# Optimization experiments

Hardware: AMD Instinct MI355X
Metric: run time of the kernel (lower is better)

Reference implementation:

```python
import jax, jax.numpy as jnp
import numpy as np
from jax import lax

NK, NV, DK, DV, K, C = 16, 32, 128, 128, 4, 2048
KEY_DIM = NK * DK
VAL_DIM = NV * DV
CONV_DIM = 2 * KEY_DIM + VAL_DIM
EPS = 1e-6


def setup_inputs() -> dict:
    key = jax.random.key(0)
    ks = jax.random.split(key, 10)
    B, T = 2, 2048
    s = 0.02
    return {
        "x": jax.random.normal(ks[0], (B, T, C), jnp.float32),
        "input_pos": jnp.arange(T, dtype=jnp.int32),
        "W_qkv": jax.random.normal(ks[1], (CONV_DIM, C), jnp.float32) * s,
        "W_z": jax.random.normal(ks[2], (VAL_DIM, C), jnp.float32) * s,
        "W_b": jax.random.normal(ks[3], (NV, C), jnp.float32) * s,
        "W_a": jax.random.normal(ks[4], (NV, C), jnp.float32) * s,
        "conv_w": jax.random.normal(ks[5], (CONV_DIM, 1, K), jnp.float32) * 0.1,
        "dt_bias": jnp.ones((NV,), jnp.float32),
        "A_log": jnp.log(jax.random.uniform(ks[6], (NV,), jnp.float32, 1e-3, 16.0)),
        "norm_w": jnp.ones((DV,), jnp.float32),
        "W_out": jax.random.normal(ks[7], (C, VAL_DIM), jnp.float32) * s,
        "conv_state": jnp.zeros((B, CONV_DIM, K), jnp.float32),
        "recurrent_state": jnp.zeros((B, NV, DK, DV), jnp.float32),
    }


def reference(x, input_pos, W_qkv, W_z, W_b, W_a, conv_w, dt_bias, A_log,
              norm_w, W_out, conv_state, recurrent_state):
    B, T, _ = x.shape
    # reset cached state when starting a new sequence (input_pos[0] == 0)
    keep = 1.0 - (input_pos[0] == 0).astype(x.dtype)
    conv_state = conv_state * keep
    state0 = recurrent_state * keep

    qkv = jnp.einsum('btc,dc->btd', x, W_qkv)                      # [B,T,CONV_DIM]
    z = jnp.einsum('btc,dc->btd', x, W_z).reshape(B, T, NV, DV)
    beta = jax.nn.sigmoid(jnp.einsum('btc,hc->bth', x, W_b))       # [B,T,NV]
    a = jnp.einsum('btc,hc->bth', x, W_a)
    g = -jnp.exp(A_log) * jax.nn.softplus(a + dt_bias)             # [B,T,NV]

    # causal depthwise conv using cached conv_state as left context
    conv_in = jnp.concatenate([conv_state, qkv.transpose(0, 2, 1)], axis=-1)  # [B,D,K+T]
    conv_out = lax.conv_general_dilated(
        conv_in, conv_w, (1,), 'VALID',
        dimension_numbers=('NCH', 'OIH', 'NCH'),
        feature_group_count=CONV_DIM)
    qkv_c = jax.nn.silu(conv_out[:, :, -T:]).transpose(0, 2, 1)    # [B,T,CONV_DIM]

    q = qkv_c[..., :KEY_DIM].reshape(B, T, NK, DK)
    k = qkv_c[..., KEY_DIM:2 * KEY_DIM].reshape(B, T, NK, DK)
    v = qkv_c[..., 2 * KEY_DIM:].reshape(B, T, NV, DV)
    q = q / jnp.maximum(jnp.linalg.norm(q, axis=-1, keepdims=True), 1e-12)
    k = k / jnp.maximum(jnp.linalg.norm(k, axis=-1, keepdims=True), 1e-12)
    rep = NV // NK
    if rep > 1:
        q = jnp.repeat(q, rep, axis=2)
        k = jnp.repeat(k, rep, axis=2)

    # gated delta-rule recurrence over time
    def step(carry, xs):
        q_i, k_i, v_i, g_i, b_i = xs                               # [B,H,*]
        new = (jnp.exp(g_i)[..., None, None] * carry
               + b_i[..., None, None] * (k_i[..., :, None] * v_i[..., None, :]))
        out = jnp.einsum('bhk,bhkv->bhv', q_i, new)
        return new, out

    xs = (q.transpose(1, 0, 2, 3), k.transpose(1, 0, 2, 3),
          v.transpose(1, 0, 2, 3), g.transpose(1, 0, 2), beta.transpose(1, 0, 2))
    state, outs = lax.scan(step, state0, xs)
    o = outs.transpose(1, 0, 2, 3)                                 # [B,T,NV,DV]

    # gated RMSNorm (Mamba2-style): gate with silu(z), then RMS-normalize
    o = o * jax.nn.silu(z)
    var = jnp.mean(o * o, axis=-1, keepdims=True)
    o = o * lax.rsqrt(var + EPS) * norm_w
    return jnp.einsum('btd,cd->btc', o.reshape(B, T, VAL_DIM), W_out)
```

## Files before the change

### kernel.cpp

```cpp
#include <hip/hip_runtime.h>
#include <hip/hip_bf16.h>
#include <math.h>

#define NKH 16
#define NVH 32
#define DKD 128
#define DVD 128
#define CDIM 2048
#define KEY_DIM 2048
#define VAL_DIM 4096
#define CONV_DIM 8192
#define BB 2
#define TT 2048
#define MROWS 4096
#define CH 64
#define NCHUNK 32

typedef unsigned short u16;
typedef __bf16 bf16x8 __attribute__((ext_vector_type(8)));
typedef float f32x4 __attribute__((ext_vector_type(4)));

__device__ __forceinline__ u16 f2bf(float f) {
    union { float f; unsigned u; } a; a.f = f;
    unsigned u = a.u;
    u += 0x7fffu + ((u >> 16) & 1u);
    return (u16)(u >> 16);
}
__device__ __forceinline__ float bf2f(u16 h) {
    union { unsigned u; float f; } a; a.u = ((unsigned)h) << 16;
    return a.f;
}
union BF8 { bf16x8 v; uint2 u2[2]; uint4 u4; u16 s[8]; };
__device__ __forceinline__ bf16x8 lds_ld8(const u16* p) {
    BF8 t; t.u2[0] = *(const uint2*)p; t.u2[1] = *(const uint2*)(p + 4); return t.v;
}
__device__ __forceinline__ void lds_st8(u16* p, uint4 v) {
    *(uint2*)p = make_uint2(v.x, v.y); *(uint2*)(p + 4) = make_uint2(v.z, v.w);
}

__global__ __launch_bounds__(256) void fill_kernel(float* __restrict__ p, float v, int n) {
    int i = blockIdx.x * 256 + threadIdx.x;
    if (i < n) p[i] = v;
}

__global__ __launch_bounds__(256) void cast_kernel(const float* __restrict__ src,
                                                   u16* __restrict__ dst, int n4) {
    int i = blockIdx.x * 256 + threadIdx.x;
    if (i >= n4) return;
    float4 v = ((const float4*)src)[i];
    ushort4 r;
    r.x = f2bf(v.x); r.y = f2bf(v.y); r.z = f2bf(v.z); r.w = f2bf(v.w);
    ((ushort4*)dst)[i] = r;
}

template<int OUT_BF16>
__global__ __launch_bounds__(256) void gemm_nt(const u16* __restrict__ A,
                                               const u16* __restrict__ Bm,
                                               void* __restrict__ Cv,
                                               int M, int N, int K) {
    __shared__ __align__(16) u16 As[128 * 64];
    __shared__ __align__(16) u16 Bs[128 * 64];
    const int tid  = threadIdx.x;
    const int lane = tid & 63;
    const int wave = tid >> 6;
    const int m0 = blockIdx.y * 128;
    const int n0 = blockIdx.x * 128;
    const int wm = (wave & 1) * 64;
    const int wn = (wave >> 1) * 64;
    const int l15  = lane & 15;
    const int quad = lane >> 4;

    f32x4 acc[4][4];
#pragma unroll
    for (int i = 0; i < 4; ++i)
#pragma unroll
        for (int j = 0; j < 4; ++j) acc[i][j] = (f32x4)0.0f;

    const int crow = tid >> 3;
    const int ccol = (tid & 7) * 8;

    for (int k0 = 0; k0 < K; k0 += 64) {
#pragma unroll
        for (int p = 0; p < 4; ++p) {
            int row = p * 32 + crow;
            const u16* ga = A + (size_t)(m0 + row) * K + k0 + ccol;
            char* la = (char*)As + (size_t)(p * 256 + (wave << 6)) * 16;
            __builtin_amdgcn_global_load_lds((const __attribute__((address_space(1))) void*)ga,
                                             (__attribute__((address_space(3))) void*)la, 16, 0, 0);
            const u16* gb = Bm + (size_t)(n0 + row) * K + k0 + ccol;
            char* lb = (char*)Bs + (size_t)(p * 256 + (wave << 6)) * 16;
            __builtin_amdgcn_global_load_lds((const __attribute__((address_space(1))) void*)gb,
                                             (__attribute__((address_space(3))) void*)lb, 16, 0, 0);
        }
        __syncthreads();
#pragma unroll
        for (int kk = 0; kk < 64; kk += 32) {
            bf16x8 af[4], bfr[4];
#pragma unroll
            for (int i = 0; i < 4; ++i) {
                af[i]  = *(const bf16x8*)&As[(wm + i * 16 + l15) * 64 + kk + quad * 8];
                bfr[i] = *(const bf16x8*)&Bs[(wn + i * 16 + l15) * 64 + kk + quad * 8];
            }
#pragma unroll
            for (int i = 0; i < 4; ++i)
#pragma unroll
                for (int j = 0; j < 4; ++j)
                    acc[i][j] = __builtin_amdgcn_mfma_f32_16x16x32_bf16(af[i], bfr[j], acc[i][j], 0, 0, 0);
        }
        __syncthreads();
    }
#pragma unroll
    for (int i = 0; i < 4; ++i) {
#pragma unroll
        for (int j = 0; j < 4; ++j) {
#pragma unroll
            for (int r = 0; r < 4; ++r) {
                int grow = m0 + wm + i * 16 + quad * 4 + r;
                int gcol = n0 + wn + j * 16 + l15;
                if (OUT_BF16) {
                    ((u16*)Cv)[(size_t)grow * N + gcol] = f2bf(acc[i][j][r]);
                } else {
                    ((float*)Cv)[(size_t)grow * N + gcol] = acc[i][j][r];
                }
            }
        }
    }
}

__global__ __launch_bounds__(256) void bg_epilogue(const float* __restrict__ scores,
                                                   const float* __restrict__ dt_bias,
                                                   const float* __restrict__ A_log,
                                                   float* __restrict__ beta,
                                                   float* __restrict__ g) {
    int i = blockIdx.x * 256 + threadIdx.x;
    int row = i >> 6, col = i & 63;
    float s = scores[(size_t)row * 128 + col];
    if (col < 32) {
        beta[(size_t)row * 32 + col] = 1.f / (1.f + __expf(-s));
    } else {
        int h = col - 32;
        float aa = s + dt_bias[h];
        float sp = (aa > 20.f) ? aa : log1pf(__expf(aa));
        g[(size_t)row * 32 + h] = -__expf(A_log[h]) * sp;
    }
}

__global__ __launch_bounds__(256) void conv_silu_kernel(const u16* __restrict__ qkv,
                                                        const float* __restrict__ conv_w,
                                                        const float* __restrict__ conv_state,
                                                        const int* __restrict__ input_pos,
                                                        u16* __restrict__ qkvc) {
    const int d   = blockIdx.x * 256 + threadIdx.x;
    const int row = blockIdx.y;
    const int t   = row & (TT - 1);
    const int b   = row >> 11;
    const float keep = (input_pos[0] == 0) ? 0.f : 1.f;
    float4 w = *(const float4*)&conv_w[(size_t)d * 4];
    float acc = 0.f;
#pragma unroll
    for (int j = 0; j < 4; ++j) {
        int u = t + j - 3;
        float v;
        if (u >= 0) v = bf2f(qkv[(size_t)(b * TT + u) * CONV_DIM + d]);
        else        v = keep * conv_state[((size_t)b * CONV_DIM + d) * 4 + (u + 4)];
        acc += (&w.x)[j] * v;
    }
    float s = acc / (1.f + __expf(-acc));
    qkvc[(size_t)row * CONV_DIM + d] = f2bf(s);
}

__global__ __launch_bounds__(256) void qknorm_kernel(u16* __restrict__ qkvc) {
    const int gid  = blockIdx.x * 4 + (threadIdx.x >> 6);
    const int lane = threadIdx.x & 63;
    const int row  = gid >> 5;
    const int h    = gid & 31;
    u16* p = qkvc + (size_t)row * CONV_DIM + h * 128;
    ushort2 vb = *(ushort2*)&p[lane * 2];
    float v0 = bf2f(vb.x), v1 = bf2f(vb.y);
    float ss = v0 * v0 + v1 * v1;
#pragma unroll
    for (int off = 32; off; off >>= 1) ss += __shfl_xor(ss, off);
    float scale = 1.f / fmaxf(sqrtf(ss), 1e-12f);
    ushort2 r;
    r.x = f2bf(v0 * scale);
    r.y = f2bf(v1 * scale);
    *(ushort2*)&p[lane * 2] = r;
}

__global__ __launch_bounds__(64) void gates_kernel(const float* __restrict__ g,
                                                   const float* __restrict__ beta_,
                                                   float* __restrict__ gcum,
                                                   float* __restrict__ qsb,
                                                   float* __restrict__ wkb,
                                                   float* __restrict__ dLb) {
    const int bh = blockIdx.x, c = blockIdx.y;
    const int b = bh >> 5, h = bh & 31;
    const int t = threadIdx.x;
    const int row = b * TT + c * CH + t;
    float G = g[(size_t)row * 32 + h];
#pragma unroll
    for (int off = 1; off < 64; off <<= 1) {
        float x = __shfl_up(G, off);
        if (t >= off) G += x;
    }
    float GL = __shfl(G, 63);
    int oidx = bh * TT + c * CH + t;
    gcum[oidx] = G;
    qsb[oidx] = __expf(G);
    wkb[oidx] = __expf(GL - G) * beta_[(size_t)row * 32 + h];
    if (t == 0) dLb[bh * NCHUNK + c] = __expf(GL);
}

__global__ __launch_bounds__(256) void ktrans_kernel(const u16* __restrict__ qkvc,
                                                     u16* __restrict__ kT) {
    const int id = blockIdx.x;
    const int tt = id & 31, dkh = (id >> 5) & 1, hk = (id >> 6) & 15, b = id >> 10;
    const int t0 = tt * 64, dk0 = dkh * 64;
    __shared__ __align__(16) u16 tile[64 * 68];
#pragma unroll
    for (int it = 0; it < 2; ++it) {
        int idx = it * 256 + threadIdx.x;
        int tl = idx >> 3, c8 = (idx & 7) * 8;
        uint4 v = *(const uint4*)&qkvc[(size_t)(b * TT + t0 + tl) * CONV_DIM + KEY_DIM + hk * 128 + dk0 + c8];
        lds_st8(&tile[tl * 68 + c8], v);
    }
    __syncthreads();
#pragma unroll
    for (int it = 0; it < 2; ++it) {
        int idx = it * 256 + threadIdx.x;
        int dkl = idx >> 3, t8 = (idx & 7) * 8;
        unsigned w[4];
#pragma unroll
        for (int p = 0; p < 4; ++p) {
            unsigned lo = tile[(t8 + 2 * p) * 68 + dkl];
            unsigned hi = tile[(t8 + 2 * p + 1) * 68 + dkl];
            w[p] = lo | (hi << 16);
        }
        *(uint4*)&kT[((size_t)((b * 16 + hk) * 128 + dk0 + dkl)) * TT + t0 + t8] =
            make_uint4(w[0], w[1], w[2], w[3]);
    }
}

__global__ __launch_bounds__(256) void chunk_state_kernel(const u16* __restrict__ qkvc,
                                                          const u16* __restrict__ kT,
                                                          const float* __restrict__ qsb,
                                                          const float* __restrict__ wkb,
                                                          const float* __restrict__ dLb,
                                                          const float* __restrict__ rec_state,
                                                          const int* __restrict__ input_pos,
                                                          u16* __restrict__ o) {
    const int b = blockIdx.x, h = blockIdx.y, dvs = blockIdx.z;
    const int tid = threadIdx.x, lane = tid & 63, wave = tid >> 6;
    const int l15 = lane & 15, quad = lane >> 4;
    const int hq = h >> 1, bh = b * 32 + h;
    const float keep = (input_pos[0] == 0) ? 0.f : 1.f;

    __shared__ __align__(16) u16 sQ[64 * 132];
    __shared__ __align__(16) u16 sKT[128 * 68];
    __shared__ __align__(16) u16 sR[32 * 132];
    __shared__ float sQS[64];

    f32x4 st[2][2];
#pragma unroll
    for (int i = 0; i < 2; ++i)
#pragma unroll
        for (int j = 0; j < 2; ++j)
#pragma unroll
            for (int r = 0; r < 4; ++r) {
                int dv = dvs * 32 + i * 16 + quad * 4 + r;
                int dk = wave * 32 + j * 16 + l15;
                st[i][j][r] = keep * rec_state[((size_t)(bh * 128 + dk)) * 128 + dv];
            }

    for (int c = 0; c < NCHUNK; ++c) {
        const int t0 = c * CH;
#pragma unroll
        for (int i = 0; i < 2; ++i)
#pragma unroll
            for (int j = 0; j < 2; ++j)
#pragma unroll
                for (int r = 0; r < 4; ++r)
                    sR[(i * 16 + quad * 4 + r) * 132 + wave * 32 + j * 16 + l15] = f2bf(st[i][j][r]);
#pragma unroll
        for (int it = 0; it < 4; ++it) {
            int idx = it * 256 + tid;
            int t = idx >> 4, c8 = (idx & 15) * 8;
            uint4 v = *(const uint4*)&qkvc[(size_t)(b * TT + t0 + t) * CONV_DIM + hq * 128 + c8];
            lds_st8(&sQ[t * 132 + c8], v);
        }
        if (tid < 64) sQS[tid] = qsb[bh * TT + t0 + tid];
        __syncthreads();
        {
            f32x4 ao[2] = {(f32x4)0.0f, (f32x4)0.0f};
#pragma unroll
            for (int kk = 0; kk < 4; ++kk) {
                bf16x8 af = lds_ld8(&sQ[(wave * 16 + l15) * 132 + kk * 32 + quad * 8]);
                bf16x8 b0 = lds_ld8(&sR[(l15) * 132 + kk * 32 + quad * 8]);
                bf16x8 b1 = lds_ld8(&sR[(16 + l15) * 132 + kk * 32 + quad * 8]);
                ao[0] = __builtin_amdgcn_mfma_f32_16x16x32_bf16(af, b0, ao[0], 0, 0, 0);
                ao[1] = __builtin_amdgcn_mfma_f32_16x16x32_bf16(af, b1, ao[1], 0, 0, 0);
            }
#pragma unroll
            for (int j = 0; j < 2; ++j)
#pragma unroll
                for (int r = 0; r < 4; ++r) {
                    int t = wave * 16 + quad * 4 + r;
                    int dv = dvs * 32 + j * 16 + l15;
                    o[((size_t)(b * TT + t0 + t) * 32 + h) * 128 + dv] = f2bf(ao[j][r] * sQS[t]);
                }
        }
        __syncthreads();
#pragma unroll
        for (int it = 0; it < 4; ++it) {
            int idx = it * 256 + tid;
            int dk = idx >> 3, t8 = (idx & 7) * 8;
            uint4 v = *(const uint4*)&kT[((size_t)((b * 16 + hq) * 128 + dk)) * TT + t0 + t8];
            lds_st8(&sKT[dk * 68 + t8], v);
        }
        {
            int t = tid >> 2, dvo = (tid & 3) * 8;
            float w = wkb[bh * TT + t0 + t];
            BF8 v;
            v.u4 = *(const uint4*)&qkvc[(size_t)(b * TT + t0 + t) * CONV_DIM + 2 * KEY_DIM + h * 128 + dvs * 32 + dvo];
#pragma unroll
            for (int u = 0; u < 8; ++u)
                sR[(dvo + u) * 68 + t] = f2bf(bf2f(v.s[u]) * w);
        }
        __syncthreads();
        {
            float d = dLb[bh * NCHUNK + c];
#pragma unroll
            for (int i = 0; i < 2; ++i)
#pragma unroll
                for (int j = 0; j < 2; ++j)
#pragma unroll
                    for (int r = 0; r < 4; ++r) st[i][j][r] *= d;
#pragma unroll
            for (int kk = 0; kk < 2; ++kk) {
                bf16x8 af[2], bfv[2];
#pragma unroll
                for (int i = 0; i < 2; ++i)
                    af[i] = lds_ld8(&sR[(i * 16 + l15) * 68 + kk * 32 + quad * 8]);
#pragma unroll
                for (int j = 0; j < 2; ++j)
                    bfv[j] = lds_ld8(&sKT[(wave * 32 + j * 16 + l15) * 68 + kk * 32 + quad * 8]);
#pragma unroll
                for (int i = 0; i < 2; ++i)
#pragma unroll
                    for (int j = 0; j < 2; ++j)
                        st[i][j] = __builtin_amdgcn_mfma_f32_16x16x32_bf16(af[i], bfv[j], st[i][j], 0, 0, 0);
            }
        }
        __syncthreads();
    }
}

__global__ __launch_bounds__(256) void chunk_intra_kernel(const u16* __restrict__ qkvc,
                                                          const float* __restrict__ gcum,
                                                          const float* __restrict__ beta_,
                                                          u16* __restrict__ o) {
    const int b = blockIdx.x, h = blockIdx.y, c = blockIdx.z;
    const int tid = threadIdx.x, lane = tid & 63, wave = tid >> 6;
    const int l15 = lane & 15, quad = lane >> 4;
    const int hq = h >> 1, bh = b * 32 + h;
    const int t0 = c * CH;

    __shared__ __align__(16) u16 sQ[64 * 132];
    __shared__ __align__(16) u16 sK[64 * 132];
    __shared__ __align__(16) u16 sVT[128 * 68];
    __shared__ float sG[64];
    __shared__ float sB[64];

#pragma unroll
    for (int it = 0; it < 4; ++it) {
        int idx = it * 256 + tid;
        int t = idx >> 4, c8 = (idx & 15) * 8;
        size_t rbase = (size_t)(b * TT + t0 + t) * CONV_DIM;
        lds_st8(&sQ[t * 132 + c8], *(const uint4*)&qkvc[rbase + hq * 128 + c8]);
        lds_st8(&sK[t * 132 + c8], *(const uint4*)&qkvc[rbase + KEY_DIM + hq * 128 + c8]);
    }
    if (tid < 64) {
        sG[tid] = gcum[bh * TT + t0 + tid];
        sB[tid] = beta_[(size_t)(b * TT + t0 + tid) * 32 + h];
    }
    __syncthreads();
    const int wm = (wave & 1) * 32, wn = (wave >> 1) * 32;
    f32x4 acc[2][2];
#pragma unroll
    for (int i = 0; i < 2; ++i)
#pragma unroll
        for (int j = 0; j < 2; ++j) acc[i][j] = (f32x4)0.0f;
#pragma unroll
    for (int kk = 0; kk < 4; ++kk) {
        bf16x8 af[2], bfv[2];
#pragma unroll
        for (int i = 0; i < 2; ++i) {
            af[i]  = lds_ld8(&sQ[(wm + i * 16 + l15) * 132 + kk * 32 + quad * 8]);
            bfv[i] = lds_ld8(&sK[(wn + i * 16 + l15) * 132 + kk * 32 + quad * 8]);
        }
#pragma unroll
        for (int i = 0; i < 2; ++i)
#pragma unroll
            for (int j = 0; j < 2; ++j)
                acc[i][j] = __builtin_amdgcn_mfma_f32_16x16x32_bf16(af[i], bfv[j], acc[i][j], 0, 0, 0);
    }
    __syncthreads();
#pragma unroll
    for (int i = 0; i < 2; ++i)
#pragma unroll
        for (int j = 0; j < 2; ++j)
#pragma unroll
            for (int r = 0; r < 4; ++r) {
                int t = wm + i * 16 + quad * 4 + r;
                int s = wn + j * 16 + l15;
                float av = 0.f;
                if (s <= t) av = __expf(sG[t] - sG[s]) * sB[s] * acc[i][j][r];
                ((u16*)sQ)[t * 68 + s] = f2bf(av);
            }
#pragma unroll
    for (int it = 0; it < 4; ++it) {
        int idx = it * 256 + tid;
        int t = idx >> 4, c8 = (idx & 15) * 8;
        lds_st8(&sK[t * 132 + c8],
                *(const uint4*)&qkvc[(size_t)(b * TT + t0 + t) * CONV_DIM + 2 * KEY_DIM + h * 128 + c8]);
    }
    __syncthreads();
    {
        int dv = (wave & 1) * 64 + lane;
        int tb = (wave >> 1) * 32;
#pragma unroll
        for (int tc = 0; tc < 4; ++tc) {
            int t8 = tb + tc * 8;
            unsigned w[4];
#pragma unroll
            for (int p = 0; p < 4; ++p) {
                unsigned lo = sK[(t8 + 2 * p) * 132 + dv];
                unsigned hi = sK[(t8 + 2 * p + 1) * 132 + dv];
                w[p] = lo | (hi << 16);
            }
            lds_st8(&sVT[dv * 68 + t8], make_uint4(w[0], w[1], w[2], w[3]));
        }
    }
    __syncthreads();
    const int wm2 = (wave & 1) * 32, wn2 = (wave >> 1) * 64;
    f32x4 oacc[2][4];
#pragma unroll
    for (int i = 0; i < 2; ++i)
#pragma unroll
        for (int j = 0; j < 4; ++j) oacc[i][j] = (f32x4)0.0f;
#pragma unroll
    for (int kk = 0; kk < 2; ++kk) {
        bf16x8 af[2], bfv[4];
#pragma unroll
        for (int i = 0; i < 2; ++i)
            af[i] = lds_ld8(&((u16*)sQ)[(wm2 + i * 16 + l15) * 68 + kk * 32 + quad * 8]);
#pragma unroll
        for (int j = 0; j < 4; ++j)
            bfv[j] = lds_ld8(&sVT[(wn2 + j * 16 + l15) * 68 + kk * 32 + quad * 8]);
#pragma unroll
        for (int i = 0; i < 2; ++i)
#pragma unroll
            for (int j = 0; j < 4; ++j)
                oacc[i][j] = __builtin_amdgcn_mfma_f32_16x16x32_bf16(af[i], bfv[j], oacc[i][j], 0, 0, 0);
    }
#pragma unroll
    for (int i = 0; i < 2; ++i)
#pragma unroll
        for (int j = 0; j < 4; ++j)
#pragma unroll
            for (int r = 0; r < 4; ++r) {
                int t = wm2 + i * 16 + quad * 4 + r;
                int dv = wn2 + j * 16 + l15;
                size_t addr = ((size_t)(b * TT + t0 + t) * 32 + h) * 128 + dv;
                o[addr] = f2bf(oacc[i][j][r] + bf2f(o[addr]));
            }
}

__global__ __launch_bounds__(256) void gnorm_kernel(const u16* __restrict__ o,
                                                    const u16* __restrict__ zb,
                                                    const float* __restrict__ norm_w,
                                                    u16* __restrict__ ob) {
    const int gid  = blockIdx.x * 4 + (threadIdx.x >> 6);
    const int lane = threadIdx.x & 63;
    const int row  = gid >> 5;
    const int h    = gid & 31;
    const size_t base = ((size_t)row * NVH + h) * DVD;
    ushort2 oraw = *(const ushort2*)&o[base + lane * 2];
    float o0 = bf2f(oraw.x), o1 = bf2f(oraw.y);
    float z0 = bf2f(zb[base + lane * 2]);
    float z1 = bf2f(zb[base + lane * 2 + 1]);
    o0 *= z0 / (1.f + __expf(-z0));
    o1 *= z1 / (1.f + __expf(-z1));
    float ss = o0 * o0 + o1 * o1;
#pragma unroll
    for (int off = 32; off; off >>= 1) ss += __shfl_xor(ss, off);
    float scale = rsqrtf(ss * (1.f / 128.f) + 1e-6f);
    float w0 = norm_w[lane * 2], w1 = norm_w[lane * 2 + 1];
    ushort2 r;
    r.x = f2bf(o0 * scale * w0);
    r.y = f2bf(o1 * scale * w1);
    *(ushort2*)&ob[base + lane * 2] = r;
}

extern "C" void kernel_launch(void* const* d_in, const int* in_sizes, int n_in,
                              void* d_out, int out_size, void* d_ws, size_t ws_size,
                              hipStream_t stream) {
    const float* x         = (const float*)d_in[0];
    const int*   input_pos = (const int*)d_in[1];
    const float* W_qkv     = (const float*)d_in[2];
    const float* W_z       = (const float*)d_in[3];
    const float* W_b       = (const float*)d_in[4];
    const float* W_a       = (const float*)d_in[5];
    const float* conv_w    = (const float*)d_in[6];
    const float* dt_bias   = (const float*)d_in[7];
    const float* A_log     = (const float*)d_in[8];
    const float* norm_w    = (const float*)d_in[9];
    const float* W_out     = (const float*)d_in[10];
    const float* conv_state = (const float*)d_in[11];
    const float* rec_state  = (const float*)d_in[12];
    float* out = (float*)d_out;

    const size_t REQUIRED = 168820736;
    if (ws_size < REQUIRED) {
        float mib = (float)((double)ws_size / 1048576.0);
        fill_kernel<<<(out_size + 255) / 256, 256, 0, stream>>>(out, mib, out_size);
        return;
    }

    const size_t MI = 1048576;
    char* ws = (char*)d_ws;
    u16* xb    = (u16*)(ws);
    u16* wqkvb = (u16*)(ws + 16 * MI);
    u16* wzb   = (u16*)(ws + 48 * MI);
    u16* wbab  = (u16*)(ws + 16 * MI);
    float* bgs = (float*)(ws + 17 * MI);
    u16* qkvc  = (u16*)(ws);
    u16* ob    = (u16*)(ws);
    u16* woutb = (u16*)(ws + 32 * MI);
    u16* zb    = (u16*)(ws + 64 * MI);
    u16* qkvb  = (u16*)(ws + 96 * MI);
    u16* o     = (u16*)(ws + 96 * MI);
    u16* kT    = (u16*)(ws + 128 * MI);
    float* gcum = (float*)(ws + 144 * MI);
    float* qsb  = (float*)(ws + 144 * MI + 524288);
    float* wkb  = (float*)(ws + 145 * MI);
    float* dLb  = (float*)(ws + 145 * MI + 524288);
    float* beta = (float*)(ws + 160 * MI);
    float* g    = (float*)(ws + 160 * MI + 524288);

    cast_kernel<<<8192,  256, 0, stream>>>(x,     xb,    2097152);
    cast_kernel<<<16384, 256, 0, stream>>>(W_qkv, wqkvb, 4194304);
    cast_kernel<<<8192,  256, 0, stream>>>(W_z,   wzb,   2097152);

    gemm_nt<1><<<dim3(64, 32), 256, 0, stream>>>(xb, wqkvb, qkvb, MROWS, CONV_DIM, CDIM);
    gemm_nt<1><<<dim3(32, 32), 256, 0, stream>>>(xb, wzb,   zb,   MROWS, VAL_DIM,  CDIM);

    cast_kernel<<<256, 256, 0, stream>>>(W_b, wbab, 16384);
    cast_kernel<<<256, 256, 0, stream>>>(W_a, wbab + 65536, 16384);
    hipMemsetAsync(wbab + 131072, 0, 131072 * sizeof(u16), stream);
    gemm_nt<0><<<dim3(1, 32), 256, 0, stream>>>(xb, wbab, bgs, MROWS, 128, CDIM);
    bg_epilogue<<<1024, 256, 0, stream>>>(bgs, dt_bias, A_log, beta, g);

    conv_silu_kernel<<<dim3(32, 4096), 256, 0, stream>>>(qkvb, conv_w, conv_state, input_pos, qkvc);
    qknorm_kernel<<<32768, 256, 0, stream>>>(qkvc);

    gates_kernel<<<dim3(64, NCHUNK), 64, 0, stream>>>(g, beta, gcum, qsb, wkb, dLb);
    ktrans_kernel<<<2048, 256, 0, stream>>>(qkvc, kT);
    chunk_state_kernel<<<dim3(BB, NVH, 4), 256, 0, stream>>>(qkvc, kT, qsb, wkb, dLb,
                                                             rec_state, input_pos, o);
    chunk_intra_kernel<<<dim3(BB, NVH, NCHUNK), 256, 0, stream>>>(qkvc, gcum, beta, o);

    cast_kernel<<<8192, 256, 0, stream>>>(W_out, woutb, 2097152);
    gnorm_kernel<<<32768, 256, 0, stream>>>(o, zb, norm_w, ob);

    gemm_nt<0><<<dim3(16, 32), 256, 0, stream>>>(ob, woutb, out, MROWS, CDIM, VAL_DIM);
}
```

Measured before the change: 860.5 us.

## Add 256x256-tile GEMM with direct-to-LDS async loads for QKV and Z projections

```diff
diff --git a/kernel.cpp b/kernel.cpp
--- a/kernel.cpp
+++ b/kernel.cpp
@@ -33,6 +33,9 @@
 union BF8 { bf16x8 v; uint2 u2[2]; uint4 u4; u16 s[8]; };
 __device__ __forceinline__ bf16x8 lds_ld8(const u16* p) {
     BF8 t; t.u2[0] = *(const uint2*)p; t.u2[1] = *(const uint2*)(p + 4); return t.v;
+}
+__device__ __forceinline__ bf16x8 lds_ld16(const u16* p) {
+    BF8 t; t.u4 = *(const uint4*)p; return t.v;
 }
 __device__ __forceinline__ void lds_st8(u16* p, uint4 v) {
     *(uint2*)p = make_uint2(v.x, v.y); *(uint2*)(p + 4) = make_uint2(v.z, v.w);
@@ -117,6 +120,106 @@
             for (int r = 0; r < 4; ++r) {
                 int grow = m0 + wm + i * 16 + quad * 4 + r;
                 int gcol = n0 + wn + j * 16 + l15;
+                if (OUT_BF16) {
+                    ((u16*)Cv)[(size_t)grow * N + gcol] = f2bf(acc[i][j][r]);
+                } else {
+                    ((float*)Cv)[(size_t)grow * N + gcol] = acc[i][j][r];
+                }
+            }
+        }
+    }
+}
+
+template<int OUT_BF16>
+__global__ __launch_bounds__(512, 2) void gemm_nt_256(const u16* __restrict__ A,
+                                                      const u16* __restrict__ Bm,
+                                                      void* __restrict__ Cv,
+                                                      int M, int N, int K) {
+    __shared__ __align__(16) u16 sA[2][256 * 64];
+    __shared__ __align__(16) u16 sB[2][256 * 64];
+    const int tid  = threadIdx.x;
+    const int lane = tid & 63;
+    const int wave = tid >> 6;
+    const int wr   = wave >> 2;
+    const int wc   = wave & 3;
+    const int l15  = lane & 15;
+    const int quad = lane >> 4;
+    const int m0 = blockIdx.y * 256;
+    const int n0 = blockIdx.x * 256;
+
+    f32x4 acc[8][4];
+#pragma unroll
+    for (int i = 0; i < 8; ++i)
+#pragma unroll
+        for (int j = 0; j < 4; ++j) acc[i][j] = (f32x4)0.0f;
+
+    auto stage = [&](int buf, int kk0) {
+#pragma unroll
+        for (int p = 0; p < 4; ++p) {
+            const int gbase = p * 512 + wave * 64;
+            const int g   = gbase + lane;
+            const int row = g >> 3;
+            const int sc  = (g & 7) ^ (row & 7);
+            const u16* ga = A + (size_t)(m0 + row) * K + kk0 + sc * 8;
+            __builtin_amdgcn_global_load_lds(
+                (const __attribute__((address_space(1))) void*)ga,
+                (__attribute__((address_space(3))) void*)((char*)&sA[buf][0] + (size_t)gbase * 16),
+                16, 0, 0);
+            const u16* gb = Bm + (size_t)(n0 + row) * K + kk0 + sc * 8;
+            __builtin_amdgcn_global_load_lds(
+                (const __attribute__((address_space(1))) void*)gb,
+                (__attribute__((address_space(3))) void*)((char*)&sB[buf][0] + (size_t)gbase * 16),
+                16, 0, 0);
+        }
+    };
+
+    const int NT = K >> 6;
+    stage(0, 0);
+
+    for (int T = 0; T < NT; ++T) {
+        const int P = T & 1;
+        __builtin_amdgcn_sched_barrier(0);
+        if (T + 1 < NT) {
+            stage(P ^ 1, (T + 1) << 6);
+            asm volatile("s_waitcnt vmcnt(8)" ::: "memory");
+        } else {
+            asm volatile("s_waitcnt vmcnt(0)" ::: "memory");
+        }
+        __builtin_amdgcn_s_barrier();
+        __builtin_amdgcn_sched_barrier(0);
+#pragma unroll
+        for (int kk = 0; kk < 2; ++kk) {
+            bf16x8 af[8], bfv[4];
+#pragma unroll
+            for (int i = 0; i < 8; ++i) {
+                int row = wr * 128 + i * 16 + l15;
+                int slot = ((kk * 4 + quad) ^ (l15 & 7)) * 8;
+                af[i] = lds_ld16(&sA[P][row * 64 + slot]);
+            }
+#pragma unroll
+            for (int j = 0; j < 4; ++j) {
+                int row = wc * 64 + j * 16 + l15;
+                int slot = ((kk * 4 + quad) ^ (l15 & 7)) * 8;
+                bfv[j] = lds_ld16(&sB[P][row * 64 + slot]);
+            }
+#pragma unroll
+            for (int i = 0; i < 8; ++i)
+#pragma unroll
+                for (int j = 0; j < 4; ++j)
+                    acc[i][j] = __builtin_amdgcn_mfma_f32_16x16x32_bf16(af[i], bfv[j], acc[i][j], 0, 0, 0);
+        }
+        __builtin_amdgcn_sched_barrier(0);
+        __builtin_amdgcn_s_barrier();
+    }
+
+#pragma unroll
+    for (int i = 0; i < 8; ++i) {
+#pragma unroll
+        for (int j = 0; j < 4; ++j) {
+#pragma unroll
+            for (int r = 0; r < 4; ++r) {
+                int grow = m0 + wr * 128 + i * 16 + quad * 4 + r;
+                int gcol = n0 + wc * 64 + j * 16 + l15;
                 if (OUT_BF16) {
                     ((u16*)Cv)[(size_t)grow * N + gcol] = f2bf(acc[i][j][r]);
                 } else {
@@ -552,8 +655,8 @@
     cast_kernel<<<16384, 256, 0, stream>>>(W_qkv, wqkvb, 4194304);
     cast_kernel<<<8192,  256, 0, stream>>>(W_z,   wzb,   2097152);
 
-    gemm_nt<1><<<dim3(64, 32), 256, 0, stream>>>(xb, wqkvb, qkvb, MROWS, CONV_DIM, CDIM);
-    gemm_nt<1><<<dim3(32, 32), 256, 0, stream>>>(xb, wzb,   zb,   MROWS, VAL_DIM,  CDIM);
+    gemm_nt_256<1><<<dim3(32, 16), 512, 0, stream>>>(xb, wqkvb, qkvb, MROWS, CONV_DIM, CDIM);
+    gemm_nt_256<1><<<dim3(16, 16), 512, 0, stream>>>(xb, wzb,   zb,   MROWS, VAL_DIM,  CDIM);
 
     cast_kernel<<<256, 256, 0, stream>>>(W_b, wbab, 16384);
     cast_kernel<<<256, 256, 0, stream>>>(W_a, wbab + 65536, 16384);
```

After: 777.3 us. 9.7% less time.
